# Optimization experiments

Measured on AMD Instinct MI355X. Metric: run time of the kernel, lower is better.

## Reference

```python
import jax, jax.numpy as jnp
import numpy as np

B, D, R = 16384, 4096, 64       # batch tokens, embed_dim, low_rank_dimension
N_PART = 8                       # number of subspace partitions
P = R // N_PART                  # partition size = 8
N_SEL = 4                        # partitions selected per example


def setup_inputs() -> dict:
    key = jax.random.key(0)
    k1, k2, k3, k4 = jax.random.split(key, 4)
    base = jax.random.normal(k1, (B, D), dtype=jnp.float32)
    source = jax.random.normal(k2, (B, D), dtype=jnp.float32)
    # orthogonal low-rank rotation (torch.nn.utils.parametrizations.orthogonal)
    W, _ = jnp.linalg.qr(jax.random.normal(k3, (D, R), dtype=jnp.float32))  # [D, R], orthonormal cols
    subspaces = jax.random.randint(k4, (B, N_SEL), 0, N_PART)               # partition ids per example
    return {"base": base, "source": source, "W": W, "subspaces": subspaces}


def reference(base, source, W, subspaces):
    # rotate into low-rank space: [B, R]
    rotated_base = base @ W
    rotated_source = source @ W
    diff = rotated_source - rotated_base

    # per-example selected rotated-space indices (contiguous partitions of size P)
    # idx[b] = concat over selected partitions of [p*P, p*P+P)
    idx = (subspaces[:, :, None] * P + jnp.arange(P)).reshape(B, N_SEL * P)  # [B, N_SEL*P]

    # Selecting columns of diff and matching rows of W.T, then matmul, is
    # equivalent to masking unselected rotated dims to zero and doing one GEMM.
    mask = jnp.zeros((B, R), dtype=diff.dtype).at[jnp.arange(B)[:, None], idx].set(1.0)
    output = base + (diff * mask) @ W.T  # [B, D]
    return output.astype(base.dtype)
```

## Files before the change

### kernel.cpp

```cpp
#include <hip/hip_runtime.h>


#define D_DIM 4096
#define R_DIM 64
#define BM    16
#define KC    64
#define KW    1024

typedef short bf16vec8 __attribute__((ext_vector_type(8)));
typedef float f32x4v  __attribute__((ext_vector_type(4)));

#define OFF_BASE    0
#define OFF_STAGE   131072
#define OFF_SCRATCH 139264
#define OFF_RM      155648
#define SMEM_BYTES  157696

__device__ __forceinline__ unsigned int f2bf_u(float f) {
  unsigned int u = __builtin_bit_cast(unsigned int, f);
  return (u + 0x7fffu + ((u >> 16) & 1u)) >> 16;
}
__device__ __forceinline__ unsigned int pack2bf(float a, float b) {
  return f2bf_u(a) | (f2bf_u(b) << 16);
}
__device__ __forceinline__ float bfbits2f(unsigned short s) {
  unsigned int u = ((unsigned int)s) << 16;
  return __builtin_bit_cast(float, u);
}

__global__ __launch_bounds__(256)
void lrri_prep(const float* __restrict__ W, unsigned short* __restrict__ Wt,
               unsigned short* __restrict__ Wb) {
  const int idx = blockIdx.x * blockDim.x + threadIdx.x;
  const int k = idx >> 4;
  const int j = (idx & 15) * 4;
  float4 w = *(const float4*)(W + (size_t)k * R_DIM + j);
  ushort4 p;
  p.x = (unsigned short)f2bf_u(w.x);
  p.y = (unsigned short)f2bf_u(w.y);
  p.z = (unsigned short)f2bf_u(w.z);
  p.w = (unsigned short)f2bf_u(w.w);
  *(ushort4*)(Wb + (size_t)k * R_DIM + j) = p;
  Wt[(size_t)(j + 0) * D_DIM + k] = p.x;
  Wt[(size_t)(j + 1) * D_DIM + k] = p.y;
  Wt[(size_t)(j + 2) * D_DIM + k] = p.z;
  Wt[(size_t)(j + 3) * D_DIM + k] = p.w;
}

template<bool USE_WS>
__global__ __launch_bounds__(256)
void lrri_fused(const float* __restrict__ base, const float* __restrict__ srcp,
                const float* __restrict__ W, const int* __restrict__ subs,
                const unsigned short* __restrict__ Wt_bf,
                const unsigned short* __restrict__ Wb_bf,
                float* __restrict__ out)
{
  __shared__ __align__(16) unsigned char smem[SMEM_BYTES];
  const int tid  = threadIdx.x;
  const int wave = tid >> 6;
  const int lane = tid & 63;
  const int l4   = lane & 15;
  const int g    = lane >> 4;
  const long rowbase = (long)blockIdx.x * BM;

  unsigned short* stage   = (unsigned short*)(smem + OFF_STAGE + wave * 2048);
  unsigned short* baseLds = (unsigned short*)(smem + OFF_BASE);

  f32x4v acc[4];
  #pragma unroll
  for (int t = 0; t < 4; ++t) acc[t] = (f32x4v){0.f, 0.f, 0.f, 0.f};

  const int kw0 = wave * KW;
  #pragma unroll 1
  for (int c = 0; c < KW / KC; ++c) {
    const int kbase = kw0 + c * KC;
    float4 b4[4], s4[4];
    #pragma unroll
    for (int i = 0; i < 4; ++i) {
      const int r = g + i * 4;
      const long off = (rowbase + r) * D_DIM + kbase + l4 * 4;
      b4[i] = *(const float4*)(base + off);
      s4[i] = *(const float4*)(srcp + off);
    }
    #pragma unroll
    for (int i = 0; i < 4; ++i) {
      const int r = g + i * 4;
      uint2 dp, bp;
      dp.x = pack2bf(s4[i].x - b4[i].x, s4[i].y - b4[i].y);
      dp.y = pack2bf(s4[i].z - b4[i].z, s4[i].w - b4[i].w);
      *(uint2*)((unsigned char*)stage + r * 128 + l4 * 8) = dp;
      bp.x = pack2bf(b4[i].x, b4[i].y);
      bp.y = pack2bf(b4[i].z, b4[i].w);
      *(uint2*)((unsigned char*)baseLds + r * 8192 + (kbase + l4 * 4) * 2) = bp;
    }
    uint4 af[2];
    #pragma unroll
    for (int s = 0; s < 2; ++s)
      af[s] = *(const uint4*)((unsigned char*)stage + l4 * 128 + s * 64 + g * 16);
    #pragma unroll
    for (int t = 0; t < 4; ++t) {
      #pragma unroll
      for (int s = 0; s < 2; ++s) {
        uint4 bfrag;
        if (USE_WS) {
          bfrag = *(const uint4*)(Wt_bf + (size_t)(t * 16 + l4) * D_DIM +
                                  kbase + s * 32 + g * 8);
        } else {
          unsigned int p[4];
          #pragma unroll
          for (int e2 = 0; e2 < 4; ++e2) {
            float wa = W[(size_t)(kbase + s * 32 + g * 8 + e2 * 2    ) * R_DIM + t * 16 + l4];
            float wb = W[(size_t)(kbase + s * 32 + g * 8 + e2 * 2 + 1) * R_DIM + t * 16 + l4];
            p[e2] = pack2bf(wa, wb);
          }
          bfrag.x = p[0]; bfrag.y = p[1]; bfrag.z = p[2]; bfrag.w = p[3];
        }
        acc[t] = __builtin_amdgcn_mfma_f32_16x16x32_bf16(
            __builtin_bit_cast(bf16vec8, af[s]),
            __builtin_bit_cast(bf16vec8, bfrag), acc[t], 0, 0, 0);
      }
    }
  }
  {
    float* part = (float*)(smem + OFF_SCRATCH + wave * 4096);
    #pragma unroll
    for (int t = 0; t < 4; ++t)
      #pragma unroll
      for (int i = 0; i < 4; ++i)
        part[(g * 4 + i) * 64 + t * 16 + l4] = acc[t][i];
  }
  __syncthreads();

  {
    const int row = tid >> 4, jg = tid & 15;
    const float* p0 = (const float*)(smem + OFF_SCRATCH);
    int4 sb = *(const int4*)(subs + (rowbase + row) * 4);
    unsigned mbits = (1u << sb.x) | (1u << sb.y) | (1u << sb.z) | (1u << sb.w);
    unsigned short vals[4];
    #pragma unroll
    for (int jj = 0; jj < 4; ++jj) {
      const int j = jg * 4 + jj;
      float sum = p0[row * 64 + j] + p0[1024 + row * 64 + j] +
                  p0[2048 + row * 64 + j] + p0[3072 + row * 64 + j];
      vals[jj] = ((mbits >> (j >> 3)) & 1u) ? (unsigned short)f2bf_u(sum)
                                            : (unsigned short)0;
    }
    unsigned short* rm = (unsigned short*)(smem + OFF_RM);
    uint2 pk;
    pk.x = (unsigned)vals[0] | ((unsigned)vals[1] << 16);
    pk.y = (unsigned)vals[2] | ((unsigned)vals[3] << 16);
    *(uint2*)(rm + row * 64 + jg * 4) = pk;
  }
  __syncthreads();

  uint4 a2[2];
  {
    const unsigned short* rm = (const unsigned short*)(smem + OFF_RM);
    #pragma unroll
    for (int s = 0; s < 2; ++s)
      a2[s] = *(const uint4*)((const unsigned char*)rm + l4 * 128 + s * 64 + g * 16);
  }
  float* cbuf = (float*)(smem + OFF_SCRATCH + wave * 4096);
  #pragma unroll 1
  for (int grp = 0; grp < 16; ++grp) {
    const int cbase = wave * 1024 + grp * 64;
    #pragma unroll
    for (int t = 0; t < 4; ++t) {
      f32x4v a = (f32x4v){0.f, 0.f, 0.f, 0.f};
      #pragma unroll
      for (int s = 0; s < 2; ++s) {
        uint4 bfrag;
        if (USE_WS) {
          bfrag = *(const uint4*)(Wb_bf + (size_t)(cbase + t * 16 + l4) * R_DIM +
                                  s * 32 + g * 8);
        } else {
          const float* wp = W + (size_t)(cbase + t * 16 + l4) * R_DIM + s * 32 + g * 8;
          float4 wa = *(const float4*)(wp);
          float4 wb = *(const float4*)(wp + 4);
          bfrag.x = pack2bf(wa.x, wa.y); bfrag.y = pack2bf(wa.z, wa.w);
          bfrag.z = pack2bf(wb.x, wb.y); bfrag.w = pack2bf(wb.z, wb.w);
        }
        a = __builtin_amdgcn_mfma_f32_16x16x32_bf16(
            __builtin_bit_cast(bf16vec8, a2[s]),
            __builtin_bit_cast(bf16vec8, bfrag), a, 0, 0, 0);
      }
      #pragma unroll
      for (int i = 0; i < 4; ++i)
        cbuf[(g * 4 + i) * 64 + t * 16 + l4] = a[i];
    }
    #pragma unroll
    for (int s2 = 0; s2 < 4; ++s2) {
      const int r = g + s2 * 4;
      f32x4v cv = *(const f32x4v*)(cbuf + r * 64 + l4 * 4);
      ushort4 bb = *(const ushort4*)((const unsigned char*)baseLds + r * 8192 +
                                     (cbase + l4 * 4) * 2);
      float4 o;
      o.x = cv[0] + bfbits2f(bb.x);
      o.y = cv[1] + bfbits2f(bb.y);
      o.z = cv[2] + bfbits2f(bb.z);
      o.w = cv[3] + bfbits2f(bb.w);
      *(float4*)(out + (rowbase + r) * D_DIM + cbase + l4 * 4) = o;
    }
  }
}

extern "C" void kernel_launch(void* const* d_in, const int* in_sizes, int n_in,
                              void* d_out, int out_size, void* d_ws, size_t ws_size,
                              hipStream_t stream) {
  const float* base = (const float*)d_in[0];
  const float* srcp = (const float*)d_in[1];
  const float* W    = (const float*)d_in[2];
  const int*   subs = (const int*)d_in[3];
  float* out = (float*)d_out;

  const int nblocks = 16384 / BM;
  const size_t wbytes = (size_t)2 * R_DIM * D_DIM * sizeof(unsigned short);
  if (d_ws && ws_size >= wbytes) {
    unsigned short* Wt = (unsigned short*)d_ws;
    unsigned short* Wb = Wt + (size_t)R_DIM * D_DIM;
    lrri_prep<<<256, 256, 0, stream>>>(W, Wt, Wb);
    lrri_fused<true><<<nblocks, 256, 0, stream>>>(base, srcp, W, subs, Wt, Wb, out);
  } else {
    lrri_fused<false><<<nblocks, 256, 0, stream>>>(base, srcp, W, subs, nullptr, nullptr, out);
  }
}
```

Before: 231.3 us.

## Shrink row tile to 4 rows per block to cut LDS and raise occupancy

Reduces the block row tile from 16 to 4. This shrinks the LDS footprint from about 157KB to 40KB, so several blocks can be resident per CU, and the launch bound now requests 4 blocks. The MFMA tiles stay 16 rows wide with 12 rows zero-padded, so three quarters of the matrix work is wasted and W is re-read per block four times as often. It also pads the LDS row strides (4104 and 72) to avoid bank conflicts.

```diff
diff --git a/kernel.cpp b/kernel.cpp
--- a/kernel.cpp
+++ b/kernel.cpp
@@ -3,18 +3,19 @@
 
 #define D_DIM 4096
 #define R_DIM 64
-#define BM    16
+#define BM    4
 #define KC    64
 #define KW    1024
+#define BASE_STRIDE 4104
 
 typedef short bf16vec8 __attribute__((ext_vector_type(8)));
 typedef float f32x4v  __attribute__((ext_vector_type(4)));
 
 #define OFF_BASE    0
-#define OFF_STAGE   131072
-#define OFF_SCRATCH 139264
-#define OFF_RM      155648
-#define SMEM_BYTES  157696
+#define OFF_STAGE   32832
+#define OFF_SCRATCH 34880
+#define OFF_RM      39488
+#define SMEM_BYTES  40000
 
 __device__ __forceinline__ unsigned int f2bf_u(float f) {
   unsigned int u = __builtin_bit_cast(unsigned int, f);
@@ -48,7 +49,7 @@
 }
 
 template<bool USE_WS>
-__global__ __launch_bounds__(256)
+__global__ __launch_bounds__(256, 4)
 void lrri_fused(const float* __restrict__ base, const float* __restrict__ srcp,
                 const float* __restrict__ W, const int* __restrict__ subs,
                 const unsigned short* __restrict__ Wt_bf,
@@ -63,7 +64,7 @@
   const int g    = lane >> 4;
   const long rowbase = (long)blockIdx.x * BM;
 
-  unsigned short* stage   = (unsigned short*)(smem + OFF_STAGE + wave * 2048);
+  unsigned short* stage   = (unsigned short*)(smem + OFF_STAGE + wave * 512);
   unsigned short* baseLds = (unsigned short*)(smem + OFF_BASE);
 
   f32x4v acc[4];
@@ -74,29 +75,22 @@
   #pragma unroll 1
   for (int c = 0; c < KW / KC; ++c) {
     const int kbase = kw0 + c * KC;
-    float4 b4[4], s4[4];
-    #pragma unroll
-    for (int i = 0; i < 4; ++i) {
-      const int r = g + i * 4;
-      const long off = (rowbase + r) * D_DIM + kbase + l4 * 4;
-      b4[i] = *(const float4*)(base + off);
-      s4[i] = *(const float4*)(srcp + off);
+    const long off = (rowbase + g) * D_DIM + kbase + l4 * 4;
+    float4 b4 = *(const float4*)(base + off);
+    float4 s4 = *(const float4*)(srcp + off);
+    uint2 dp, bp;
+    dp.x = pack2bf(s4.x - b4.x, s4.y - b4.y);
+    dp.y = pack2bf(s4.z - b4.z, s4.w - b4.w);
+    *(uint2*)((unsigned char*)stage + g * 128 + l4 * 8) = dp;
+    bp.x = pack2bf(b4.x, b4.y);
+    bp.y = pack2bf(b4.z, b4.w);
+    *(uint2*)((unsigned char*)baseLds + g * (BASE_STRIDE * 2) + (kbase + l4 * 4) * 2) = bp;
+
+    uint4 af0 = {0u, 0u, 0u, 0u}, af1 = {0u, 0u, 0u, 0u};
+    if (l4 < BM) {
+      af0 = *(const uint4*)((unsigned char*)stage + l4 * 128 + 0 * 64 + g * 16);
+      af1 = *(const uint4*)((unsigned char*)stage + l4 * 128 + 1 * 64 + g * 16);
     }
-    #pragma unroll
-    for (int i = 0; i < 4; ++i) {
-      const int r = g + i * 4;
-      uint2 dp, bp;
-      dp.x = pack2bf(s4[i].x - b4[i].x, s4[i].y - b4[i].y);
-      dp.y = pack2bf(s4[i].z - b4[i].z, s4[i].w - b4[i].w);
-      *(uint2*)((unsigned char*)stage + r * 128 + l4 * 8) = dp;
-      bp.x = pack2bf(b4[i].x, b4[i].y);
-      bp.y = pack2bf(b4[i].z, b4[i].w);
-      *(uint2*)((unsigned char*)baseLds + r * 8192 + (kbase + l4 * 4) * 2) = bp;
-    }
-    uint4 af[2];
-    #pragma unroll
-    for (int s = 0; s < 2; ++s)
-      af[s] = *(const uint4*)((unsigned char*)stage + l4 * 128 + s * 64 + g * 16);
     #pragma unroll
     for (int t = 0; t < 4; ++t) {
       #pragma unroll
@@ -116,51 +110,41 @@
           bfrag.x = p[0]; bfrag.y = p[1]; bfrag.z = p[2]; bfrag.w = p[3];
         }
         acc[t] = __builtin_amdgcn_mfma_f32_16x16x32_bf16(
-            __builtin_bit_cast(bf16vec8, af[s]),
+            __builtin_bit_cast(bf16vec8, s == 0 ? af0 : af1),
             __builtin_bit_cast(bf16vec8, bfrag), acc[t], 0, 0, 0);
       }
     }
   }
-  {
-    float* part = (float*)(smem + OFF_SCRATCH + wave * 4096);
+  if (g == 0) {
+    float* part = (float*)(smem + OFF_SCRATCH + wave * 1152);
     #pragma unroll
     for (int t = 0; t < 4; ++t)
       #pragma unroll
       for (int i = 0; i < 4; ++i)
-        part[(g * 4 + i) * 64 + t * 16 + l4] = acc[t][i];
+        part[i * 72 + t * 16 + l4] = acc[t][i];
   }
   __syncthreads();
 
   {
-    const int row = tid >> 4, jg = tid & 15;
+    const int row = tid >> 6, j = tid & 63;
     const float* p0 = (const float*)(smem + OFF_SCRATCH);
+    float sum = p0[row * 72 + j] + p0[288 + row * 72 + j] +
+                p0[576 + row * 72 + j] + p0[864 + row * 72 + j];
     int4 sb = *(const int4*)(subs + (rowbase + row) * 4);
     unsigned mbits = (1u << sb.x) | (1u << sb.y) | (1u << sb.z) | (1u << sb.w);
-    unsigned short vals[4];
-    #pragma unroll
-    for (int jj = 0; jj < 4; ++jj) {
-      const int j = jg * 4 + jj;
-      float sum = p0[row * 64 + j] + p0[1024 + row * 64 + j] +
-                  p0[2048 + row * 64 + j] + p0[3072 + row * 64 + j];
-      vals[jj] = ((mbits >> (j >> 3)) & 1u) ? (unsigned short)f2bf_u(sum)
-                                            : (unsigned short)0;
-    }
-    unsigned short* rm = (unsigned short*)(smem + OFF_RM);
-    uint2 pk;
-    pk.x = (unsigned)vals[0] | ((unsigned)vals[1] << 16);
-    pk.y = (unsigned)vals[2] | ((unsigned)vals[3] << 16);
-    *(uint2*)(rm + row * 64 + jg * 4) = pk;
+    unsigned short v = ((mbits >> (j >> 3)) & 1u) ? (unsigned short)f2bf_u(sum)
+                                                  : (unsigned short)0;
+    ((unsigned short*)(smem + OFF_RM))[row * 64 + j] = v;
   }
   __syncthreads();
 
-  uint4 a2[2];
-  {
-    const unsigned short* rm = (const unsigned short*)(smem + OFF_RM);
-    #pragma unroll
-    for (int s = 0; s < 2; ++s)
-      a2[s] = *(const uint4*)((const unsigned char*)rm + l4 * 128 + s * 64 + g * 16);
-  }
-  float* cbuf = (float*)(smem + OFF_SCRATCH + wave * 4096);
+  uint4 a20 = {0u, 0u, 0u, 0u}, a21 = {0u, 0u, 0u, 0u};
+  if (l4 < BM) {
+    const unsigned char* rm = smem + OFF_RM;
+    a20 = *(const uint4*)(rm + l4 * 128 + 0 * 64 + g * 16);
+    a21 = *(const uint4*)(rm + l4 * 128 + 1 * 64 + g * 16);
+  }
+  float* cbuf = (float*)(smem + OFF_SCRATCH + wave * 1152);
   #pragma unroll 1
   for (int grp = 0; grp < 16; ++grp) {
     const int cbase = wave * 1024 + grp * 64;
@@ -181,26 +165,24 @@
           bfrag.z = pack2bf(wb.x, wb.y); bfrag.w = pack2bf(wb.z, wb.w);
         }
         a = __builtin_amdgcn_mfma_f32_16x16x32_bf16(
-            __builtin_bit_cast(bf16vec8, a2[s]),
+            __builtin_bit_cast(bf16vec8, s == 0 ? a20 : a21),
             __builtin_bit_cast(bf16vec8, bfrag), a, 0, 0, 0);
       }
-      #pragma unroll
-      for (int i = 0; i < 4; ++i)
-        cbuf[(g * 4 + i) * 64 + t * 16 + l4] = a[i];
+      if (g == 0) {
+        #pragma unroll
+        for (int i = 0; i < 4; ++i)
+          cbuf[i * 72 + t * 16 + l4] = a[i];
+      }
     }
-    #pragma unroll
-    for (int s2 = 0; s2 < 4; ++s2) {
-      const int r = g + s2 * 4;
-      f32x4v cv = *(const f32x4v*)(cbuf + r * 64 + l4 * 4);
-      ushort4 bb = *(const ushort4*)((const unsigned char*)baseLds + r * 8192 +
-                                     (cbase + l4 * 4) * 2);
-      float4 o;
-      o.x = cv[0] + bfbits2f(bb.x);
-      o.y = cv[1] + bfbits2f(bb.y);
-      o.z = cv[2] + bfbits2f(bb.z);
-      o.w = cv[3] + bfbits2f(bb.w);
-      *(float4*)(out + (rowbase + r) * D_DIM + cbase + l4 * 4) = o;
-    }
+    f32x4v cv = *(const f32x4v*)(cbuf + g * 72 + l4 * 4);
+    ushort4 bb = *(const ushort4*)((const unsigned char*)baseLds +
+                                   g * (BASE_STRIDE * 2) + (cbase + l4 * 4) * 2);
+    float4 o;
+    o.x = cv[0] + bfbits2f(bb.x);
+    o.y = cv[1] + bfbits2f(bb.y);
+    o.z = cv[2] + bfbits2f(bb.z);
+    o.w = cv[3] + bfbits2f(bb.w);
+    *(float4*)(out + (rowbase + g) * D_DIM + cbase + l4 * 4) = o;
   }
 }
 
```

New measurement: 515.4 us. 2.23x slower.
